# Performance work log

Measured on AMD Instinct MI355X. Metric: run time of the kernel, lower is better.

## Reference

```python
import jax, jax.numpy as jnp
import numpy as np


def setup_inputs() -> dict:
    key = jax.random.key(0)
    ks = jax.random.split(key, 4)
    B, D, H, W, C = 1, 24, 24, 24, 256
    C_ = C // 8
    x = jax.random.normal(ks[0], (B, D, H, W, C), dtype=jnp.float32)
    # 1x1x1 Conv3D kernels are just [C_in, C_out] matrices (glorot-ish scale)
    wg = jax.random.normal(ks[1], (C, C_), dtype=jnp.float32) * (1.0 / np.sqrt(C))
    wf = jax.random.normal(ks[2], (C, C_), dtype=jnp.float32) * (1.0 / np.sqrt(C))
    wh = jax.random.normal(ks[3], (C, C), dtype=jnp.float32) * (1.0 / np.sqrt(C))
    bg = jnp.zeros((C_,), dtype=jnp.float32)
    bf = jnp.zeros((C_,), dtype=jnp.float32)
    bh = jnp.zeros((C,), dtype=jnp.float32)
    gamma = jnp.zeros((C,), dtype=jnp.float32)  # module initializes gamma to zeros
    return {"x": x, "wg": wg, "bg": bg, "wf": wf, "bf": bf, "wh": wh, "bh": bh, "gamma": gamma}


def reference(x, wg, bg, wf, bf, wh, bh, gamma):
    B, D, H, W, C = x.shape
    N = D * H * W
    xt = x.reshape(B, N, C)                      # [B, N, C] tokens
    x_g = jnp.einsum('bnc,cf->bnf', xt, wg) + bg  # [B, N, C_] (query)
    x_f = jnp.einsum('bnc,cf->bnf', xt, wf) + bf  # [B, N, C_] (key)
    x_h = jnp.einsum('bnc,cd->bnd', xt, wh) + bh  # [B, N, C]  (value)
    s = jnp.einsum('bnf,bmf->bnm', x_g, x_f)      # [B, N, N] scores
    s = jax.nn.softmax(s, axis=-1)
    o = jnp.einsum('bnm,bmd->bnd', s, x_h)        # [B, N, C]
    o = o.reshape(B, D, H, W, C)
    return gamma * o + x
```

## Files before the change

### kernel.cpp

```cpp
#include <hip/hip_runtime.h>
#include <math.h>

#define N_TOK 13824
#define KT 32
#define LOG2E 1.44269504088896f

typedef __attribute__((ext_vector_type(8)))  short bf16x8;
typedef __attribute__((ext_vector_type(4)))  float f32x4;
typedef __attribute__((ext_vector_type(16))) float f32x16;
typedef unsigned short u16;

#define AS3(p) ((__attribute__((address_space(3))) void*)(p))
#define AS1(p) ((const __attribute__((address_space(1))) void*)(p))
#define GLL(gp, lp) __builtin_amdgcn_global_load_lds(AS1(gp), AS3(lp), 16, 0, 0)

__device__ inline u16 f2b(float v) {
    union { float f; unsigned u; } a; a.f = v;
    unsigned r = a.u + 0x7fffu + ((a.u >> 16) & 1u);
    return (u16)(r >> 16);
}
__device__ inline float b2f(u16 v) {
    union { unsigned u; float f; } a; a.u = ((unsigned)v) << 16; return a.f;
}
__device__ inline float dev_exp2(float x) {
    float r;
    asm volatile("v_exp_f32 %0, %1" : "=v"(r) : "v"(x));
    return r;
}
__device__ inline float cross_max(float v) {
    float a = v, b = v;
    asm volatile("v_permlane32_swap_b32 %0, %1" : "+v"(a), "+v"(b));
    return fmaxf(a, b);
}
__device__ inline float cross_sum(float v) {
    float a = v, b = v;
    asm volatile("v_permlane32_swap_b32 %0, %1" : "+v"(a), "+v"(b));
    return a + b;
}
__device__ inline unsigned cvtpk(float lo, float hi) {
    unsigned r;
    asm volatile("v_cvt_pk_bf16_f32 %0, %1, %2" : "=v"(r) : "v"(lo), "v"(hi));
    return r;
}

__global__ __launch_bounds__(512) void prep_kernel(
    const float* __restrict__ x, const float* __restrict__ wh,
    const float* __restrict__ wg, const float* __restrict__ wf,
    u16* __restrict__ xb, u16* __restrict__ wt)
{
    int id = blockIdx.x * 512 + threadIdx.x;
    if (id < N_TOK * 256 / 4) {
        float4 v = ((const float4*)x)[id];
        ushort4 o;
        o.x = f2b(v.x); o.y = f2b(v.y); o.z = f2b(v.z); o.w = f2b(v.w);
        ((ushort4*)xb)[id] = o;
    }
    if (id < 320 * 256) {
        int n = id >> 8, k = id & 255;
        float v = (n < 256) ? wh[k * 256 + n]
                : (n < 288) ? wg[k * 32 + (n - 256)] * LOG2E
                            : wf[k * 32 + (n - 288)];
        wt[n * 256 + k] = f2b(v);
    }
}

__global__ __launch_bounds__(256) void proj_kernel(
    const u16* __restrict__ xb, const u16* __restrict__ wt,
    const float* __restrict__ bg, const float* __restrict__ bfv, const float* __restrict__ bh,
    u16* __restrict__ g, u16* __restrict__ f, u16* __restrict__ h)
{
    __shared__ u16 As[64 * 64];
    __shared__ u16 Bs[64 * 64];
    const int t = threadIdx.x, l = t & 63, w = t >> 6;
    const int m0 = blockIdx.x * 64, n0 = blockIdx.y * 64;
    const int mh = (w & 1) * 32, nh = (w >> 1) * 32;
    f32x4 acc[2][2] = {};

    for (int kstep = 0; kstep < 4; ++kstep) {
        const int k0 = kstep * 64;
        __syncthreads();
        #pragma unroll
        for (int i = 0; i < 2; ++i) {
            int ch  = w * 2 + i;
            int row = ch * 8 + (l >> 3);
            int ul  = (l & 7) ^ ((l >> 3) & 7);
            GLL(xb + (size_t)(m0 + row) * 256 + k0 + ul * 8, As + ch * 512);
            GLL(wt + (size_t)(n0 + row) * 256 + k0 + ul * 8, Bs + ch * 512);
        }
        asm volatile("s_waitcnt vmcnt(0)" ::: "memory");
        __syncthreads();
        #pragma unroll
        for (int ks = 0; ks < 2; ++ks) {
            bf16x8 a[2], b[2];
            #pragma unroll
            for (int mf = 0; mf < 2; ++mf) {
                int row = mh + mf * 16 + (l & 15);
                int u   = (ks * 4 + (l >> 4)) ^ (row & 7);
                a[mf] = *(const bf16x8*)(As + row * 64 + u * 8);
            }
            #pragma unroll
            for (int nf = 0; nf < 2; ++nf) {
                int row = nh + nf * 16 + (l & 15);
                int u   = (ks * 4 + (l >> 4)) ^ (row & 7);
                b[nf] = *(const bf16x8*)(Bs + row * 64 + u * 8);
            }
            #pragma unroll
            for (int mf = 0; mf < 2; ++mf)
                #pragma unroll
                for (int nf = 0; nf < 2; ++nf)
                    acc[mf][nf] = __builtin_amdgcn_mfma_f32_16x16x32_bf16(
                        a[mf], b[nf], acc[mf][nf], 0, 0, 0);
        }
    }

    #pragma unroll
    for (int mf = 0; mf < 2; ++mf)
        #pragma unroll
        for (int nf = 0; nf < 2; ++nf)
            #pragma unroll
            for (int r = 0; r < 4; ++r) {
                int row = m0 + mh + mf * 16 + (l >> 4) * 4 + r;
                int col = n0 + nh + nf * 16 + (l & 15);
                float bias = (col < 256) ? bh[col]
                           : (col < 288) ? bg[col - 256] * LOG2E
                                         : bfv[col - 288];
                u16 v = f2b(acc[mf][nf][r] + bias);
                if (col < 256)      h[(size_t)row * 256 + col] = v;
                else if (col < 288) g[(size_t)row * 32 + (col - 256)] = v;
                else                f[(size_t)row * 32 + (col - 288)] = v;
            }
}

__global__ __launch_bounds__(256) void transpose_kernel(
    const u16* __restrict__ h, u16* __restrict__ ht)
{
    __shared__ u16 tile[64][65];
    const int t = threadIdx.x;
    const int r0 = blockIdx.x * 64, c0 = blockIdx.y * 64;
    #pragma unroll
    for (int i = 0; i < 16; ++i) {
        int r = i * 4 + (t >> 6), c = t & 63;
        tile[r][c] = h[(size_t)(r0 + r) * 256 + c0 + c];
    }
    __syncthreads();
    #pragma unroll
    for (int i = 0; i < 16; ++i) {
        int c = i * 4 + (t >> 6), r = t & 63;
        ht[(size_t)(c0 + c) * N_TOK + r0 + r] = tile[r][c];
    }
}

__global__ __launch_bounds__(256, 2) void attn_kernel(
    const u16* __restrict__ g, const u16* __restrict__ f, const u16* __restrict__ ht,
    u16* __restrict__ po, float* __restrict__ pm, float* __restrict__ pl,
    int kps, int ntiles)
{
    __shared__ u16 VtF[2 * 8192];
    __shared__ u16 KsF[2 * 1024];
    __shared__ float rfs[4][32];

    const int t = threadIdx.x, l = t & 63, w = t >> 6;
    const int hi = l >> 5, l31 = l & 31;
    const int q0 = blockIdx.x * 128 + w * 32;
    const int kbase = blockIdx.y * kps;

    bf16x8 qf[2];
    #pragma unroll
    for (int ks = 0; ks < 2; ++ks)
        qf[ks] = *(const bf16x8*)(g + (size_t)(q0 + l31) * 32 + ks * 16 + hi * 8);

    f32x16 acc[8] = {};
    float m_run = -1e30f, l_run = 0.f;

    int voffV[4];
    #pragma unroll
    for (int i = 0; i < 4; ++i) {
        int u = i * 256 + t;
        int ch = u >> 2, gg = u & 3, kg = gg ^ ((ch >> 1) & 3);
        voffV[i] = ch * N_TOK + kg * 8;
    }
    int koffK = 0;
    { int key = (t & 127) >> 2, gcu = t & 3, cu = gcu ^ ((key >> 1) & 3);
      koffK = key * 32 + cu * 8; }

    const int sw = (l31 >> 1) & 3;
    int rbase[2];
    #pragma unroll
    for (int ks = 0; ks < 2; ++ks)
        rbase[ks] = (l31 * 4 + ((2 * ks + hi) ^ sw)) * 8;

    auto stage = [&](int tile, int db) {
        const u16* vsrc = ht + kbase + tile * KT;
        #pragma unroll
        for (int i = 0; i < 4; ++i)
            GLL(vsrc + voffV[i], &VtF[db * 8192 + (i * 256 + t) * 8]);
        if (t < 128)
            GLL(f + (size_t)(kbase + tile * KT) * 32 + koffK, &KsF[db * 1024 + t * 8]);
    };

    stage(0, 0);

    for (int tl = 0; tl < ntiles; tl += 2) {
        #pragma unroll
        for (int sub = 0; sub < 2; ++sub) {
            const int b = sub, cur = tl + sub;
            asm volatile("" ::: "memory");
            __builtin_amdgcn_s_barrier();
            asm volatile("" ::: "memory");
            { int nx = cur + 1 < ntiles ? cur + 1 : 0; stage(nx, b ^ 1); }
            if (w < 2) asm volatile("s_waitcnt vmcnt(5)" ::: "memory");
            else       asm volatile("s_waitcnt vmcnt(4)" ::: "memory");
            __builtin_amdgcn_s_barrier();
            asm volatile("" ::: "memory");

            bf16x8 kf0 = *(const bf16x8*)&KsF[b * 1024 + rbase[0]];
            bf16x8 kf1 = *(const bf16x8*)&KsF[b * 1024 + rbase[1]];

            f32x16 z = {};
            z = __builtin_amdgcn_mfma_f32_32x32x16_bf16(kf0, qf[0], z, 0, 0, 0);
            f32x16 s = __builtin_amdgcn_mfma_f32_32x32x16_bf16(kf1, qf[1], z, 0, 0, 0);

            float m1 = fmaxf(fmaxf(s[0], s[1]), s[2]);
            float m2 = fmaxf(fmaxf(s[3], s[4]), s[5]);
            float m3 = fmaxf(fmaxf(s[6], s[7]), s[8]);
            float m4 = fmaxf(fmaxf(s[9], s[10]), s[11]);
            float m5 = fmaxf(fmaxf(s[12], s[13]), s[14]);
            float mA = fmaxf(fmaxf(m1, m2), m3);
            float mB = fmaxf(fmaxf(m4, m5), s[15]);
            float mrow = cross_max(fmaxf(mA, mB));

            if (!__all(mrow <= m_run + 11.54f)) {
                float mnew = fmaxf(m_run, mrow);
                float rf = dev_exp2(m_run - mnew);
                m_run = mnew;
                l_run *= rf;
                if (hi == 0) rfs[w][l31] = rf;
                asm volatile("s_waitcnt lgkmcnt(0)" ::: "memory");
                __builtin_amdgcn_sched_barrier(0);
                float4 rv[4];
                #pragma unroll
                for (int bb = 0; bb < 4; ++bb)
                    rv[bb] = *(const float4*)&rfs[w][bb * 8 + hi * 4];
                #pragma unroll
                for (int cht = 0; cht < 8; ++cht)
                    #pragma unroll
                    for (int r = 0; r < 16; ++r)
                        acc[cht][r] *= rv[r >> 2][r & 3];
            }
            float pv[16];
            #pragma unroll
            for (int r = 0; r < 16; ++r) pv[r] = dev_exp2(s[r] - m_run);
            float s8[8];
            #pragma unroll
            for (int i = 0; i < 8; ++i) s8[i] = pv[i] + pv[i + 8];
            float s4a = s8[0] + s8[1], s4b = s8[2] + s8[3];
            float s4c = s8[4] + s8[5], s4d = s8[6] + s8[7];
            l_run += (s4a + s4b) + (s4c + s4d);

            unsigned pa[2][4];
            #pragma unroll
            for (int ks = 0; ks < 2; ++ks) {
                const int o = ks * 8;
                unsigned a0 = cvtpk(pv[o + 0], pv[o + 1]);
                unsigned b0 = cvtpk(pv[o + 2], pv[o + 3]);
                unsigned a1 = cvtpk(pv[o + 4], pv[o + 5]);
                unsigned b1 = cvtpk(pv[o + 6], pv[o + 7]);
                asm volatile("v_permlane32_swap_b32 %0, %1" : "+v"(a0), "+v"(a1));
                asm volatile("v_permlane32_swap_b32 %0, %1" : "+v"(b0), "+v"(b1));
                pa[ks][0] = a0; pa[ks][1] = b0;
                pa[ks][2] = a1; pa[ks][3] = b1;
            }

            __builtin_amdgcn_s_setprio(1);
            #pragma unroll
            for (int ks = 0; ks < 2; ++ks) {
                union { unsigned u[4]; bf16x8 v; } pb;
                pb.u[0] = pa[ks][0]; pb.u[1] = pa[ks][1];
                pb.u[2] = pa[ks][2]; pb.u[3] = pa[ks][3];
                #pragma unroll
                for (int cht = 0; cht < 8; ++cht) {
                    bf16x8 vf = *(const bf16x8*)&VtF[b * 8192 + cht * 1024 + rbase[ks]];
                    acc[cht] = __builtin_amdgcn_mfma_f32_32x32x16_bf16(
                        pb.v, vf, acc[cht], 0, 0, 0);
                }
            }
            __builtin_amdgcn_s_setprio(0);
        }
    }

    const int split = blockIdx.y;
    #pragma unroll
    for (int cht = 0; cht < 8; ++cht) {
        int ch = cht * 32 + l31;
        #pragma unroll
        for (int r = 0; r < 16; ++r) {
            int qq = q0 + (r & 3) + 8 * (r >> 2) + 4 * hi;
            po[((size_t)split * N_TOK + qq) * 256 + ch] = f2b(acc[cht][r]);
        }
    }
    float lfull = cross_sum(l_run);
    if (hi == 0) {
        int qq = q0 + l31;
        pm[(size_t)split * N_TOK + qq] = m_run;
        pl[(size_t)split * N_TOK + qq] = lfull;
    }
}

__global__ __launch_bounds__(256) void combine_kernel(
    const u16* __restrict__ po, const float* __restrict__ pm, const float* __restrict__ pl,
    const float* __restrict__ x, const float* __restrict__ gamma, float* __restrict__ out,
    int nsplit)
{
    const int t = threadIdx.x;
    const int q = blockIdx.x * 4 + (t >> 6);
    const int c4 = (t & 63) * 4;

    float M = -1e30f;
    for (int s = 0; s < nsplit; ++s) M = fmaxf(M, pm[(size_t)s * N_TOK + q]);
    float lsum = 0.f, o0 = 0.f, o1 = 0.f, o2 = 0.f, o3 = 0.f;
    for (int s = 0; s < nsplit; ++s) {
        float wsc = dev_exp2(pm[(size_t)s * N_TOK + q] - M);
        lsum += wsc * pl[(size_t)s * N_TOK + q];
        ushort4 p4 = *(const ushort4*)(po + ((size_t)s * N_TOK + q) * 256 + c4);
        o0 += wsc * b2f(p4.x); o1 += wsc * b2f(p4.y);
        o2 += wsc * b2f(p4.z); o3 += wsc * b2f(p4.w);
    }
    float inv = 1.f / lsum;
    float4 gm = *(const float4*)(gamma + c4);
    float4 xv = *(const float4*)(x + (size_t)q * 256 + c4);
    float4 ov;
    ov.x = gm.x * (o0 * inv) + xv.x;
    ov.y = gm.y * (o1 * inv) + xv.y;
    ov.z = gm.z * (o2 * inv) + xv.z;
    ov.w = gm.w * (o3 * inv) + xv.w;
    *(float4*)(out + (size_t)q * 256 + c4) = ov;
}

extern "C" void kernel_launch(void* const* d_in, const int* in_sizes, int n_in,
                              void* d_out, int out_size, void* d_ws, size_t ws_size,
                              hipStream_t stream) {
    const float* x     = (const float*)d_in[0];
    const float* wg    = (const float*)d_in[1];
    const float* bg    = (const float*)d_in[2];
    const float* wf    = (const float*)d_in[3];
    const float* bfv   = (const float*)d_in[4];
    const float* wh    = (const float*)d_in[5];
    const float* bh    = (const float*)d_in[6];
    const float* gamma = (const float*)d_in[7];
    float* out = (float*)d_out;

    const size_t base_b = (size_t)N_TOK * 640;
    auto need = [&](int ns) {
        return base_b + (size_t)ns * N_TOK * 512 + (size_t)ns * N_TOK * 8 + 1024;
    };
    int nsplit = 4;
    if (ws_size >= need(9)) nsplit = 9;
    else if (ws_size >= need(6)) nsplit = 6;
    const int kps = N_TOK / nsplit, ntiles = kps / KT;

    u16* ws = (u16*)d_ws;
    u16* gq = ws;
    u16* fk = gq + (size_t)N_TOK * 32;
    u16* ht = fk + (size_t)N_TOK * 32;
    u16* po = ht + (size_t)N_TOK * 256;
    u16* xb = po;
    u16* wt = xb + (size_t)N_TOK * 256;
    u16* hv = wt + 320 * 256;
    float* pm = (float*)(po + (size_t)nsplit * N_TOK * 256);
    float* pl = pm + (size_t)nsplit * N_TOK;

    prep_kernel<<<1728, 512, 0, stream>>>(x, wh, wg, wf, xb, wt);
    proj_kernel<<<dim3(216, 5), 256, 0, stream>>>(xb, wt, bg, bfv, bh, gq, fk, hv);
    transpose_kernel<<<dim3(216, 4), 256, 0, stream>>>(hv, ht);
    attn_kernel<<<dim3(108, nsplit), 256, 0, stream>>>(gq, fk, ht, po, pm, pl, kps, ntiles);
    combine_kernel<<<N_TOK / 4, 256, 0, stream>>>(po, pm, pl, x, gamma, out, nsplit);
}
```

Baseline: 169.7 us.

## Split attention value channels across grid z and double key tile size

The attention kernel now splits the 256 value channels into two halves over a new grid z dimension, so each block keeps 4 accumulator tiles instead of 8. This lowers register pressure and allows 3 blocks per CU. The key tile grows from 32 to 64 keys. Keys are now loaded straight from global memory into registers and double-buffered across sub-iterations instead of being staged through LDS. The trade-off is that QK^T scores and the softmax exponentials are computed twice, once per channel half.

```diff
diff --git a/kernel.cpp b/kernel.cpp
--- a/kernel.cpp
+++ b/kernel.cpp
@@ -2,7 +2,7 @@
 #include <math.h>
 
 #define N_TOK 13824
-#define KT 32
+#define KT 64
 #define LOG2E 1.44269504088896f
 
 typedef __attribute__((ext_vector_type(8)))  short bf16x8;
@@ -150,75 +150,81 @@
     }
 }
 
-__global__ __launch_bounds__(256, 2) void attn_kernel(
-    const u16* __restrict__ g, const u16* __restrict__ f, const u16* __restrict__ ht,
+__global__ __launch_bounds__(256, 3) void attn_kernel(
+    const u16* __restrict__ g, const u16* __restrict__ fk, const u16* __restrict__ ht,
     u16* __restrict__ po, float* __restrict__ pm, float* __restrict__ pl,
     int kps, int ntiles)
 {
     __shared__ u16 VtF[2 * 8192];
-    __shared__ u16 KsF[2 * 1024];
     __shared__ float rfs[4][32];
 
     const int t = threadIdx.x, l = t & 63, w = t >> 6;
     const int hi = l >> 5, l31 = l & 31;
     const int q0 = blockIdx.x * 128 + w * 32;
+    const int z  = blockIdx.z;
     const int kbase = blockIdx.y * kps;
 
-    bf16x8 qf[2];
-    #pragma unroll
-    for (int ks = 0; ks < 2; ++ks)
-        qf[ks] = *(const bf16x8*)(g + (size_t)(q0 + l31) * 32 + ks * 16 + hi * 8);
-
-    f32x16 acc[8] = {};
+    bf16x8 qf0 = *(const bf16x8*)(g + (size_t)(q0 + l31) * 32 + hi * 8);
+    bf16x8 qf1 = *(const bf16x8*)(g + (size_t)(q0 + l31) * 32 + 16 + hi * 8);
+
+    f32x16 acc[4] = {};
     float m_run = -1e30f, l_run = 0.f;
 
-    int voffV[4];
+    const u16* vbase = ht + (size_t)(z * 128) * N_TOK + kbase;
+    int voff[4];
     #pragma unroll
     for (int i = 0; i < 4; ++i) {
         int u = i * 256 + t;
-        int ch = u >> 2, gg = u & 3, kg = gg ^ ((ch >> 1) & 3);
-        voffV[i] = ch * N_TOK + kg * 8;
-    }
-    int koffK = 0;
-    { int key = (t & 127) >> 2, gcu = t & 3, cu = gcu ^ ((key >> 1) & 3);
-      koffK = key * 32 + cu * 8; }
-
-    const int sw = (l31 >> 1) & 3;
-    int rbase[2];
-    #pragma unroll
-    for (int ks = 0; ks < 2; ++ks)
-        rbase[ks] = (l31 * 4 + ((2 * ks + hi) ^ sw)) * 8;
-
-    auto stage = [&](int tile, int db) {
-        const u16* vsrc = ht + kbase + tile * KT;
+        int ch = u >> 3, gg = u & 7, kg = gg ^ (ch & 7);
+        voff[i] = ch * N_TOK + kg * 8;
+    }
+    const u16* ksrc = fk + (size_t)kbase * 32 + l31 * 32 + hi * 8;
+
+    const int swv = l31 & 7;
+    int rbase[4];
+    #pragma unroll
+    for (int ks16 = 0; ks16 < 4; ++ks16)
+        rbase[ks16] = l31 * 64 + (((ks16 * 2 + hi) ^ swv)) * 8;
+
+    auto stageV = [&](int tile, int db) {
+        const u16* vs = vbase + tile * KT;
         #pragma unroll
         for (int i = 0; i < 4; ++i)
-            GLL(vsrc + voffV[i], &VtF[db * 8192 + (i * 256 + t) * 8]);
-        if (t < 128)
-            GLL(f + (size_t)(kbase + tile * KT) * 32 + koffK, &KsF[db * 1024 + t * 8]);
+            GLL(vs + voff[i], &VtF[db * 8192 + (i * 256 + t) * 8]);
     };
-
-    stage(0, 0);
-
-    for (int tl = 0; tl < ntiles; tl += 2) {
-        #pragma unroll
-        for (int sub = 0; sub < 2; ++sub) {
-            const int b = sub, cur = tl + sub;
-            asm volatile("" ::: "memory");
-            __builtin_amdgcn_s_barrier();
-            asm volatile("" ::: "memory");
-            { int nx = cur + 1 < ntiles ? cur + 1 : 0; stage(nx, b ^ 1); }
-            if (w < 2) asm volatile("s_waitcnt vmcnt(5)" ::: "memory");
-            else       asm volatile("s_waitcnt vmcnt(4)" ::: "memory");
-            __builtin_amdgcn_s_barrier();
-            asm volatile("" ::: "memory");
-
-            bf16x8 kf0 = *(const bf16x8*)&KsF[b * 1024 + rbase[0]];
-            bf16x8 kf1 = *(const bf16x8*)&KsF[b * 1024 + rbase[1]];
-
-            f32x16 z = {};
-            z = __builtin_amdgcn_mfma_f32_32x32x16_bf16(kf0, qf[0], z, 0, 0, 0);
-            f32x16 s = __builtin_amdgcn_mfma_f32_32x32x16_bf16(kf1, qf[1], z, 0, 0, 0);
+    auto loadK = [&](int tile, bf16x8& k0, bf16x8& k1, bf16x8& k2, bf16x8& k3) {
+        const u16* kp = ksrc + (size_t)tile * KT * 32;
+        k0 = *(const bf16x8*)(kp);
+        k1 = *(const bf16x8*)(kp + 16);
+        k2 = *(const bf16x8*)(kp + 1024);
+        k3 = *(const bf16x8*)(kp + 1040);
+    };
+
+    bf16x8 kA0, kA1, kA2, kA3, kB0, kB1, kB2, kB3;
+    stageV(0, 0);
+    loadK(0, kA0, kA1, kA2, kA3);
+
+    auto sub = [&](int b, int cur,
+                   bf16x8 k0, bf16x8 k1, bf16x8 k2, bf16x8 k3,
+                   bf16x8& n0, bf16x8& n1, bf16x8& n2, bf16x8& n3) {
+        asm volatile("" ::: "memory");
+        __builtin_amdgcn_s_barrier();
+        asm volatile("" ::: "memory");
+        int nx = cur + 1 < ntiles ? cur + 1 : 0;
+        stageV(nx, b ^ 1);
+        loadK(nx, n0, n1, n2, n3);
+        asm volatile("s_waitcnt vmcnt(8)" ::: "memory");
+        __builtin_amdgcn_s_barrier();
+        asm volatile("" ::: "memory");
+
+        #pragma unroll
+        for (int kb = 0; kb < 2; ++kb) {
+            bf16x8 kf0 = kb ? k2 : k0;
+            bf16x8 kf1 = kb ? k3 : k1;
+
+            f32x16 zz = {};
+            zz = __builtin_amdgcn_mfma_f32_32x32x16_bf16(kf0, qf0, zz, 0, 0, 0);
+            f32x16 s = __builtin_amdgcn_mfma_f32_32x32x16_bf16(kf1, qf1, s = zz, 0, 0, 0);
 
             float m1 = fmaxf(fmaxf(s[0], s[1]), s[2]);
             float m2 = fmaxf(fmaxf(s[3], s[4]), s[5]);
@@ -242,7 +248,7 @@
                 for (int bb = 0; bb < 4; ++bb)
                     rv[bb] = *(const float4*)&rfs[w][bb * 8 + hi * 4];
                 #pragma unroll
-                for (int cht = 0; cht < 8; ++cht)
+                for (int cht = 0; cht < 4; ++cht)
                     #pragma unroll
                     for (int r = 0; r < 16; ++r)
                         acc[cht][r] *= rv[r >> 2][r & 3];
@@ -274,24 +280,30 @@
             __builtin_amdgcn_s_setprio(1);
             #pragma unroll
             for (int ks = 0; ks < 2; ++ks) {
+                const int ks16 = kb * 2 + ks;
                 union { unsigned u[4]; bf16x8 v; } pb;
                 pb.u[0] = pa[ks][0]; pb.u[1] = pa[ks][1];
                 pb.u[2] = pa[ks][2]; pb.u[3] = pa[ks][3];
                 #pragma unroll
-                for (int cht = 0; cht < 8; ++cht) {
-                    bf16x8 vf = *(const bf16x8*)&VtF[b * 8192 + cht * 1024 + rbase[ks]];
+                for (int cht = 0; cht < 4; ++cht) {
+                    bf16x8 vf = *(const bf16x8*)&VtF[b * 8192 + cht * 2048 + rbase[ks16]];
                     acc[cht] = __builtin_amdgcn_mfma_f32_32x32x16_bf16(
                         pb.v, vf, acc[cht], 0, 0, 0);
                 }
             }
             __builtin_amdgcn_s_setprio(0);
         }
+    };
+
+    for (int tl = 0; tl < ntiles; tl += 2) {
+        sub(0, tl,     kA0, kA1, kA2, kA3, kB0, kB1, kB2, kB3);
+        sub(1, tl + 1, kB0, kB1, kB2, kB3, kA0, kA1, kA2, kA3);
     }
 
     const int split = blockIdx.y;
     #pragma unroll
-    for (int cht = 0; cht < 8; ++cht) {
-        int ch = cht * 32 + l31;
+    for (int cht = 0; cht < 4; ++cht) {
+        int ch = z * 128 + cht * 32 + l31;
         #pragma unroll
         for (int r = 0; r < 16; ++r) {
             int qq = q0 + (r & 3) + 8 * (r >> 2) + 4 * hi;
@@ -299,7 +311,7 @@
         }
     }
     float lfull = cross_sum(l_run);
-    if (hi == 0) {
+    if (z == 0 && hi == 0) {
         int qq = q0 + l31;
         pm[(size_t)split * N_TOK + qq] = m_run;
         pl[(size_t)split * N_TOK + qq] = lfull;
@@ -372,6 +384,6 @@
     prep_kernel<<<1728, 512, 0, stream>>>(x, wh, wg, wf, xb, wt);
     proj_kernel<<<dim3(216, 5), 256, 0, stream>>>(xb, wt, bg, bfv, bh, gq, fk, hv);
     transpose_kernel<<<dim3(216, 4), 256, 0, stream>>>(hv, ht);
-    attn_kernel<<<dim3(108, nsplit), 256, 0, stream>>>(gq, fk, ht, po, pm, pl, kps, ntiles);
+    attn_kernel<<<dim3(108, nsplit, 2), 256, 0, stream>>>(gq, fk, ht, po, pm, pl, kps, ntiles);
     combine_kernel<<<N_TOK / 4, 256, 0, stream>>>(po, pm, pl, x, gamma, out, nsplit);
 }
```

After: 196.8 us. 1.16x slower.

## Double attention key tile to 64, remap workgroups per XCD, defer row-sum

Applied to the files above, without the earlier changes.

Each pipeline stage of the flash-attention loop now covers 64 keys instead of 32, using two 32-key score MFMA blocks. This halves the barrier and staging round-trips per key, at the cost of twice the double-buffered LDS and a new 8-way V swizzle. Workgroup IDs are remapped so each XCD processes a contiguous run of (split, query-block) work, which aims to improve L2 reuse of K/V within a split. The row-sum accumulation is moved after the PV MFMAs so it can overlap with matrix work.

```diff
diff --git a/kernel.cpp b/kernel.cpp
--- a/kernel.cpp
+++ b/kernel.cpp
@@ -2,7 +2,7 @@
 #include <math.h>
 
 #define N_TOK 13824
-#define KT 32
+#define KT 64
 #define LOG2E 1.44269504088896f
 
 typedef __attribute__((ext_vector_type(8)))  short bf16x8;
@@ -151,74 +151,87 @@
 }
 
 __global__ __launch_bounds__(256, 2) void attn_kernel(
-    const u16* __restrict__ g, const u16* __restrict__ f, const u16* __restrict__ ht,
+    const u16* __restrict__ g, const u16* __restrict__ fk, const u16* __restrict__ ht,
     u16* __restrict__ po, float* __restrict__ pm, float* __restrict__ pl,
-    int kps, int ntiles)
-{
-    __shared__ u16 VtF[2 * 8192];
-    __shared__ u16 KsF[2 * 1024];
+    int kps, int ntiles, int nwg)
+{
+    __shared__ u16 VtF[2 * 16384];
+    __shared__ u16 KsF[2 * 2048];
     __shared__ float rfs[4][32];
+
+    int orig = blockIdx.x + blockIdx.y * 108;
+    int qd = nwg >> 3, rr = nwg & 7;
+    int xcd = orig & 7, idx = orig >> 3;
+    int wgid = (xcd < rr ? xcd * (qd + 1) : rr * (qd + 1) + (xcd - rr) * qd) + idx;
+    const int split = wgid / 108;
+    const int qblk  = wgid % 108;
 
     const int t = threadIdx.x, l = t & 63, w = t >> 6;
     const int hi = l >> 5, l31 = l & 31;
-    const int q0 = blockIdx.x * 128 + w * 32;
-    const int kbase = blockIdx.y * kps;
-
-    bf16x8 qf[2];
-    #pragma unroll
-    for (int ks = 0; ks < 2; ++ks)
-        qf[ks] = *(const bf16x8*)(g + (size_t)(q0 + l31) * 32 + ks * 16 + hi * 8);
+    const int q0 = qblk * 128 + w * 32;
+    const int kbase = split * kps;
+
+    bf16x8 qf0 = *(const bf16x8*)(g + (size_t)(q0 + l31) * 32 + hi * 8);
+    bf16x8 qf1 = *(const bf16x8*)(g + (size_t)(q0 + l31) * 32 + 16 + hi * 8);
 
     f32x16 acc[8] = {};
     float m_run = -1e30f, l_run = 0.f;
 
-    int voffV[4];
+    const u16* vbase = ht + kbase;
+    int voffV[8];
+    #pragma unroll
+    for (int i = 0; i < 8; ++i) {
+        int u = i * 256 + t;
+        int ch = u >> 3, gg = u & 7, kg = gg ^ (ch & 7);
+        voffV[i] = ch * N_TOK + kg * 8;
+    }
+    int koffK;
+    { int key = t >> 2, gcu = t & 3, cu = gcu ^ ((key >> 1) & 3);
+      koffK = key * 32 + cu * 8; }
+    const u16* kbp = fk + (size_t)kbase * 32;
+
+    int rbV[4];
     #pragma unroll
     for (int i = 0; i < 4; ++i) {
-        int u = i * 256 + t;
-        int ch = u >> 2, gg = u & 3, kg = gg ^ ((ch >> 1) & 3);
-        voffV[i] = ch * N_TOK + kg * 8;
-    }
-    int koffK = 0;
-    { int key = (t & 127) >> 2, gcu = t & 3, cu = gcu ^ ((key >> 1) & 3);
-      koffK = key * 32 + cu * 8; }
-
-    const int sw = (l31 >> 1) & 3;
-    int rbase[2];
+        int kg = i * 2 + hi;
+        rbV[i] = l31 * 64 + ((kg ^ (l31 & 7)) * 8);
+    }
+    int rbK[2];
     #pragma unroll
     for (int ks = 0; ks < 2; ++ks)
-        rbase[ks] = (l31 * 4 + ((2 * ks + hi) ^ sw)) * 8;
+        rbK[ks] = l31 * 4 * 8 + (((ks * 2 + hi) ^ ((l31 >> 1) & 3)) * 8);
 
     auto stage = [&](int tile, int db) {
-        const u16* vsrc = ht + kbase + tile * KT;
-        #pragma unroll
-        for (int i = 0; i < 4; ++i)
-            GLL(vsrc + voffV[i], &VtF[db * 8192 + (i * 256 + t) * 8]);
-        if (t < 128)
-            GLL(f + (size_t)(kbase + tile * KT) * 32 + koffK, &KsF[db * 1024 + t * 8]);
+        const u16* vs = vbase + tile * KT;
+        #pragma unroll
+        for (int i = 0; i < 8; ++i)
+            GLL(vs + voffV[i], &VtF[db * 16384 + (i * 256 + t) * 8]);
+        GLL(kbp + tile * (KT * 32) + koffK, &KsF[db * 2048 + t * 8]);
     };
 
     stage(0, 0);
 
-    for (int tl = 0; tl < ntiles; tl += 2) {
-        #pragma unroll
-        for (int sub = 0; sub < 2; ++sub) {
-            const int b = sub, cur = tl + sub;
-            asm volatile("" ::: "memory");
-            __builtin_amdgcn_s_barrier();
-            asm volatile("" ::: "memory");
-            { int nx = cur + 1 < ntiles ? cur + 1 : 0; stage(nx, b ^ 1); }
-            if (w < 2) asm volatile("s_waitcnt vmcnt(5)" ::: "memory");
-            else       asm volatile("s_waitcnt vmcnt(4)" ::: "memory");
-            __builtin_amdgcn_s_barrier();
-            asm volatile("" ::: "memory");
-
-            bf16x8 kf0 = *(const bf16x8*)&KsF[b * 1024 + rbase[0]];
-            bf16x8 kf1 = *(const bf16x8*)&KsF[b * 1024 + rbase[1]];
-
-            f32x16 z = {};
-            z = __builtin_amdgcn_mfma_f32_32x32x16_bf16(kf0, qf[0], z, 0, 0, 0);
-            f32x16 s = __builtin_amdgcn_mfma_f32_32x32x16_bf16(kf1, qf[1], z, 0, 0, 0);
+    auto sub = [&](int b, int cur) {
+        asm volatile("" ::: "memory");
+        __builtin_amdgcn_s_barrier();
+        asm volatile("" ::: "memory");
+        { int nx = cur + 1 < ntiles ? cur + 1 : 0; stage(nx, b ^ 1); }
+        asm volatile("s_waitcnt vmcnt(9)" ::: "memory");
+        __builtin_amdgcn_s_barrier();
+        asm volatile("" ::: "memory");
+
+        bf16x8 kf[2][2];
+        #pragma unroll
+        for (int kb = 0; kb < 2; ++kb)
+            #pragma unroll
+            for (int ks = 0; ks < 2; ++ks)
+                kf[kb][ks] = *(const bf16x8*)&KsF[b * 2048 + kb * 1024 + rbK[ks]];
+
+        #pragma unroll
+        for (int kb = 0; kb < 2; ++kb) {
+            f32x16 zz = {};
+            zz = __builtin_amdgcn_mfma_f32_32x32x16_bf16(kf[kb][0], qf0, zz, 0, 0, 0);
+            f32x16 s = __builtin_amdgcn_mfma_f32_32x32x16_bf16(kf[kb][1], qf1, zz, 0, 0, 0);
 
             float m1 = fmaxf(fmaxf(s[0], s[1]), s[2]);
             float m2 = fmaxf(fmaxf(s[3], s[4]), s[5]);
@@ -250,12 +263,6 @@
             float pv[16];
             #pragma unroll
             for (int r = 0; r < 16; ++r) pv[r] = dev_exp2(s[r] - m_run);
-            float s8[8];
-            #pragma unroll
-            for (int i = 0; i < 8; ++i) s8[i] = pv[i] + pv[i + 8];
-            float s4a = s8[0] + s8[1], s4b = s8[2] + s8[3];
-            float s4c = s8[4] + s8[5], s4d = s8[6] + s8[7];
-            l_run += (s4a + s4b) + (s4c + s4d);
 
             unsigned pa[2][4];
             #pragma unroll
@@ -279,16 +286,27 @@
                 pb.u[2] = pa[ks][2]; pb.u[3] = pa[ks][3];
                 #pragma unroll
                 for (int cht = 0; cht < 8; ++cht) {
-                    bf16x8 vf = *(const bf16x8*)&VtF[b * 8192 + cht * 1024 + rbase[ks]];
+                    bf16x8 vf = *(const bf16x8*)&VtF[b * 16384 + cht * 2048 + rbV[kb * 2 + ks]];
                     acc[cht] = __builtin_amdgcn_mfma_f32_32x32x16_bf16(
                         pb.v, vf, acc[cht], 0, 0, 0);
                 }
             }
             __builtin_amdgcn_s_setprio(0);
+
+            float s8[8];
+            #pragma unroll
+            for (int i = 0; i < 8; ++i) s8[i] = pv[i] + pv[i + 8];
+            float s4a = s8[0] + s8[1], s4b = s8[2] + s8[3];
+            float s4c = s8[4] + s8[5], s4d = s8[6] + s8[7];
+            l_run += (s4a + s4b) + (s4c + s4d);
         }
-    }
-
-    const int split = blockIdx.y;
+    };
+
+    for (int tl = 0; tl < ntiles; tl += 2) {
+        sub(0, tl);
+        sub(1, tl + 1);
+    }
+
     #pragma unroll
     for (int cht = 0; cht < 8; ++cht) {
         int ch = cht * 32 + l31;
@@ -357,6 +375,7 @@
     if (ws_size >= need(9)) nsplit = 9;
     else if (ws_size >= need(6)) nsplit = 6;
     const int kps = N_TOK / nsplit, ntiles = kps / KT;
+    const int nwg = 108 * nsplit;
 
     u16* ws = (u16*)d_ws;
     u16* gq = ws;
@@ -372,6 +391,6 @@
     prep_kernel<<<1728, 512, 0, stream>>>(x, wh, wg, wf, xb, wt);
     proj_kernel<<<dim3(216, 5), 256, 0, stream>>>(xb, wt, bg, bfv, bh, gq, fk, hv);
     transpose_kernel<<<dim3(216, 4), 256, 0, stream>>>(hv, ht);
-    attn_kernel<<<dim3(108, nsplit), 256, 0, stream>>>(gq, fk, ht, po, pm, pl, kps, ntiles);
+    attn_kernel<<<dim3(108, nsplit), 256, 0, stream>>>(gq, fk, ht, po, pm, pl, kps, ntiles, nwg);
     combine_kernel<<<N_TOK / 4, 256, 0, stream>>>(po, pm, pl, x, gamma, out, nsplit);
 }
```

Result: no change. 167.4 us (-1.3%).
